# Kernel tuning notes

Hardware: AMD Instinct MI355X
Metric: run time of the kernel (lower is better)

The kernel has to match this reference:

```python
import jax, jax.numpy as jnp
import numpy as np


def sign_ste(x):
    # forward: sign(x); backward: grad * (|x| <= 1)  (straight-through estimator)
    # clip has exactly the STE gradient mask; stop_gradient swaps in sign(x) for fwd value.
    c = jnp.clip(x, -1.0, 1.0)
    return c + jax.lax.stop_gradient(jnp.sign(x) - c)


def setup_inputs() -> dict:
    key = jax.random.key(0)
    k1, k2, k3 = jax.random.split(key, 3)
    N, CIN, COUT = 8192, 4096, 4096
    input_x = jax.random.normal(k1, (N, CIN), dtype=jnp.float32)
    weight = jax.random.normal(k2, (COUT, CIN), dtype=jnp.float32) * 0.02
    bias = jax.random.normal(k3, (COUT,), dtype=jnp.float32) * 0.01
    return {"input_x": input_x, "weight": weight, "bias": bias}


def reference(input_x, weight, bias):
    qw = sign_ste(weight)            # [COUT, CIN], values in {-1, 0, +1}
    qx = sign_ste(input_x)           # [N, CIN]
    out = jnp.einsum('nc,oc->no', qx, qw)  # binary GEMM executed as float matmul
    alpha = jnp.mean(jnp.abs(weight))
    betta = jnp.mean(jnp.abs(input_x))
    return out * alpha * betta + bias
```

## Files before the change

### kernel.cpp

```cpp
#include <hip/hip_runtime.h>
#include <stdint.h>

#define N_ROWS 8192
#define C_IN   4096
#define C_OUT  4096
#define NCHUNK (C_IN / 64)
#define MT4    65536

typedef int   v4i  __attribute__((ext_vector_type(4)));
typedef int   v8i  __attribute__((ext_vector_type(8)));
typedef float v16f __attribute__((ext_vector_type(16)));

__global__ void pack_all_kernel(const float* __restrict__ x,
                                const float* __restrict__ w,
                                uint8_t* __restrict__ xf,
                                uint8_t* __restrict__ wf,
                                float* __restrict__ partials) {
    __shared__ __align__(16) uint16_t tile16[4096];
    __shared__ float sacc[4];

    const int b = blockIdx.x;
    const float* src; uint8_t* dst; int slab;
    if (b < 2048) { src = x; dst = xf; slab = b; }
    else          { src = w; dst = wf; slab = b - 2048; }
    const int mt = slab >> 3, cg = slab & 7;

    const int t = threadIdx.x;
    const int r = t >> 3, lc = t & 7;

    const float4* base = (const float4*)(src + (size_t)(mt * 32 + r) * C_IN + cg * 512) + lc;
    float acc = 0.f;
#pragma unroll
    for (int it = 0; it < 16; ++it) {
        float4 v = base[it * 8];
        uint16_t nv = (uint16_t)((v.x > 0.f ? 0x2u : 0xAu)
                               | (v.y > 0.f ? 0x2u : 0xAu) << 4
                               | (v.z > 0.f ? 0x2u : 0xAu) << 8
                               | (v.w > 0.f ? 0x2u : 0xAu) << 12);
        acc += fabsf(v.x) + fabsf(v.y) + fabsf(v.z) + fabsf(v.w);
        tile16[it * 256 + t] = nv;
    }
    __syncthreads();
    uint4* gout = (uint4*)(dst + (size_t)mt * MT4 + (size_t)cg * 8192);
    const uint4* lin = (const uint4*)tile16;
#pragma unroll
    for (int p = 0; p < 2; ++p) gout[p * 256 + t] = lin[p * 256 + t];

    for (int off = 32; off > 0; off >>= 1) acc += __shfl_down(acc, off, 64);
    const int lane = t & 63, wv = t >> 6;
    if (lane == 0) sacc[wv] = acc;
    __syncthreads();
    if (t == 0) {
        float s = 0.f;
        for (int i = 0; i < 4; ++i) s += sacc[i];
        partials[b] = s;
    }
}

__global__ void finalize_kernel(const float* __restrict__ part_x, int nx,
                                const float* __restrict__ part_w, int nw,
                                float* __restrict__ out_ab) {
    __shared__ float s[256];
    float ax = 0.f;
    for (int i = threadIdx.x; i < nx; i += 256) ax += part_x[i];
    s[threadIdx.x] = ax; __syncthreads();
    for (int st = 128; st > 0; st >>= 1) {
        if (threadIdx.x < st) s[threadIdx.x] += s[threadIdx.x + st];
        __syncthreads();
    }
    float sumx = s[0];
    __syncthreads();
    float aw = 0.f;
    for (int i = threadIdx.x; i < nw; i += 256) aw += part_w[i];
    s[threadIdx.x] = aw; __syncthreads();
    for (int st = 128; st > 0; st >>= 1) {
        if (threadIdx.x < st) s[threadIdx.x] += s[threadIdx.x + st];
        __syncthreads();
    }
    if (threadIdx.x == 0) {
        float sumw = s[0];
        float alpha = sumw / (float)((long long)C_OUT * C_IN);
        float betta = sumx / (float)((long long)N_ROWS * C_IN);
        out_ab[0] = alpha * betta;
    }
}

#define MF(a, b, c) \
    __builtin_amdgcn_mfma_scale_f32_32x32x64_f8f6f4( \
        __builtin_shufflevector((a), (a), 0, 1, 2, 3, -1, -1, -1, -1), \
        __builtin_shufflevector((b), (b), 0, 1, 2, 3, -1, -1, -1, -1), \
        (c), 4, 4, 0, 127, 0, 127)

__launch_bounds__(512, 2)
__global__ void xnor_gemm_fp4(const uint8_t* __restrict__ Afrag,
                              const uint8_t* __restrict__ Bfrag,
                              const float* __restrict__ bias,
                              const float* __restrict__ ab_ptr,
                              float* __restrict__ out) {
    __shared__ __align__(16) uint8_t lds[4][2][8192];

    const int t    = threadIdx.x;
    const int lane = t & 63;
    const int hi   = lane >> 5;
    const int r    = lane & 31;
    const int wid  = t >> 6;
    const int wr   = wid >> 2;
    const int wc   = wid & 3;

    const int id  = blockIdx.x;
    const int swz = (id & 7) * 64 + (id >> 3);
    const int brow = (swz >> 4) * 256;
    const int bcol = (swz & 15) * 256;

    const uint8_t* Abase = Afrag + (size_t)(brow >> 5) * MT4;
    const uint8_t* Bbase = Bfrag + (size_t)(bcol >> 5) * MT4;
    const size_t soff = (size_t)(t >> 6) * MT4 + (size_t)(t & 63) * 16;

#define STG(BUF, c)                                                                     \
    do {                                                                                \
        size_t ka = (size_t)(c) * 1024;                                                 \
        __builtin_amdgcn_global_load_lds(                                               \
            (const __attribute__((address_space(1))) void*)(Abase + soff + ka),         \
            (__attribute__((address_space(3))) void*)(&lds[BUF][0][t * 16]), 16, 0, 0); \
        __builtin_amdgcn_global_load_lds(                                               \
            (const __attribute__((address_space(1))) void*)(Bbase + soff + ka),         \
            (__attribute__((address_space(3))) void*)(&lds[BUF][1][t * 16]), 16, 0, 0); \
    } while (0)

#define LOADFRAGS(AS, BS, BUF)                                                       \
    do {                                                                             \
        AS[0] = *(const v4i*)(&lds[BUF][0][((wr * 4 + 0) * 64 + lane) * 16]);        \
        AS[1] = *(const v4i*)(&lds[BUF][0][((wr * 4 + 1) * 64 + lane) * 16]);        \
        AS[2] = *(const v4i*)(&lds[BUF][0][((wr * 4 + 2) * 64 + lane) * 16]);        \
        AS[3] = *(const v4i*)(&lds[BUF][0][((wr * 4 + 3) * 64 + lane) * 16]);        \
        BS[0] = *(const v4i*)(&lds[BUF][1][((wc * 2 + 0) * 64 + lane) * 16]);        \
        BS[1] = *(const v4i*)(&lds[BUF][1][((wc * 2 + 1) * 64 + lane) * 16]);        \
    } while (0)

#define DOMFMA(AS, BS)                                \
    do {                                              \
        acc[0][0] = MF(AS[0], BS[0], acc[0][0]);      \
        acc[0][1] = MF(AS[0], BS[1], acc[0][1]);      \
        acc[1][0] = MF(AS[1], BS[0], acc[1][0]);      \
        acc[1][1] = MF(AS[1], BS[1], acc[1][1]);      \
        acc[2][0] = MF(AS[2], BS[0], acc[2][0]);      \
        acc[2][1] = MF(AS[2], BS[1], acc[2][1]);      \
        acc[3][0] = MF(AS[3], BS[0], acc[3][0]);      \
        acc[3][1] = MF(AS[3], BS[1], acc[3][1]);      \
    } while (0)

#define BODY(cexp, SBUF, NBUF, CA, CB, NA, NB)                                      \
    do {                                                                            \
        const int c_ = (cexp);                                                      \
        if (c_ + 3 < NCHUNK) STG(SBUF, c_ + 3);                                     \
        if (c_ + 1 < NCHUNK) {                                                      \
            if (c_ < NCHUNK - 3)       { asm volatile("s_waitcnt vmcnt(4)" ::: "memory"); } \
            else if (c_ == NCHUNK - 3) { asm volatile("s_waitcnt vmcnt(2)" ::: "memory"); } \
            else                       { asm volatile("s_waitcnt vmcnt(0)" ::: "memory"); } \
        }                                                                           \
        asm volatile("s_waitcnt lgkmcnt(0)" ::: "memory");                          \
        __builtin_amdgcn_s_barrier();                                               \
        if (c_ + 1 < NCHUNK) LOADFRAGS(NA, NB, NBUF);                               \
        __builtin_amdgcn_s_setprio(1);                                              \
        DOMFMA(CA, CB);                                                             \
        __builtin_amdgcn_s_setprio(0);                                              \
    } while (0)

    v16f acc[4][2] = {};
    v4i A0[4], B0[2], A1[4], B1[2];

    STG(0, 0); STG(1, 1); STG(2, 2);
    asm volatile("s_waitcnt vmcnt(4)" ::: "memory");
    __builtin_amdgcn_s_barrier();
    LOADFRAGS(A0, B0, 0);

    for (int cb = 0; cb < NCHUNK; cb += 4) {
        BODY(cb + 0, 3, 1, A0, B0, A1, B1);
        BODY(cb + 1, 0, 2, A1, B1, A0, B0);
        BODY(cb + 2, 1, 3, A0, B0, A1, B1);
        BODY(cb + 3, 2, 0, A1, B1, A0, B0);
    }

    const float ab = ab_ptr[0];
#pragma unroll
    for (int m = 0; m < 4; ++m) {
#pragma unroll
        for (int n = 0; n < 2; ++n) {
            int col = bcol + wc * 64 + n * 32 + r;
            float bv = bias[col];
#pragma unroll
            for (int reg = 0; reg < 16; ++reg) {
                int rowf = (reg & 3) + 8 * (reg >> 2) + 4 * hi;
                int grow = brow + wr * 128 + m * 32 + rowf;
                out[(size_t)grow * C_OUT + col] = acc[m][n][reg] * ab + bv;
            }
        }
    }
#undef STG
#undef LOADFRAGS
#undef DOMFMA
#undef BODY
}

extern "C" void kernel_launch(void* const* d_in, const int* in_sizes, int n_in,
                              void* d_out, int out_size, void* d_ws, size_t ws_size,
                              hipStream_t stream) {
    const float* x    = (const float*)d_in[0];
    const float* w    = (const float*)d_in[1];
    const float* bias = (const float*)d_in[2];
    float* out = (float*)d_out;

    char* ws = (char*)d_ws;
    float* red      = (float*)ws;
    float* partials = red + 16;
    uint8_t* xs  = (uint8_t*)(ws + 16384);
    uint8_t* wsg = xs + (size_t)N_ROWS * C_IN / 2;

    pack_all_kernel<<<3072, 256, 0, stream>>>(x, w, xs, wsg, partials);
    finalize_kernel<<<1, 256, 0, stream>>>(partials, 2048, partials + 2048, 1024, red);

    dim3 grid((N_ROWS / 256) * (C_OUT / 256));
    xnor_gemm_fp4<<<grid, 512, 0, stream>>>(xs, wsg, bias, red, out);
}
```

Measured before the change: 140.2 us.

## Load MFMA fragments directly from global memory, dropping LDS staging

Removes the 4-stage LDS ring buffer and its global_load_lds staging, waitcnt and barriers. Each wave now loads its own A/B fp4 fragments straight from global memory into registers, double-buffered across k-chunks. This eliminates LDS traffic and block-wide synchronisation. In exchange, A and B tiles are reloaded from global/L2 by every wave that shares them (A by 4 waves, B by 2), and the prefetch depth drops to one chunk, so load latency may be exposed.

```diff
diff --git a/kernel.cpp b/kernel.cpp
--- a/kernel.cpp
+++ b/kernel.cpp
@@ -97,8 +97,6 @@
                               const float* __restrict__ bias,
                               const float* __restrict__ ab_ptr,
                               float* __restrict__ out) {
-    __shared__ __align__(16) uint8_t lds[4][2][8192];
-
     const int t    = threadIdx.x;
     const int lane = t & 63;
     const int hi   = lane >> 5;
@@ -112,33 +110,28 @@
     const int brow = (swz >> 4) * 256;
     const int bcol = (swz & 15) * 256;
 
-    const uint8_t* Abase = Afrag + (size_t)(brow >> 5) * MT4;
-    const uint8_t* Bbase = Bfrag + (size_t)(bcol >> 5) * MT4;
-    const size_t soff = (size_t)(t >> 6) * MT4 + (size_t)(t & 63) * 16;
+    const uint8_t* pa[4];
+    const uint8_t* pb[2];
+#pragma unroll
+    for (int m = 0; m < 4; ++m)
+        pa[m] = Afrag + (size_t)((brow >> 5) + wr * 4 + m) * MT4 + (size_t)lane * 16;
+#pragma unroll
+    for (int n = 0; n < 2; ++n)
+        pb[n] = Bfrag + (size_t)((bcol >> 5) + wc * 2 + n) * MT4 + (size_t)lane * 16;
 
-#define STG(BUF, c)                                                                     \
-    do {                                                                                \
-        size_t ka = (size_t)(c) * 1024;                                                 \
-        __builtin_amdgcn_global_load_lds(                                               \
-            (const __attribute__((address_space(1))) void*)(Abase + soff + ka),         \
-            (__attribute__((address_space(3))) void*)(&lds[BUF][0][t * 16]), 16, 0, 0); \
-        __builtin_amdgcn_global_load_lds(                                               \
-            (const __attribute__((address_space(1))) void*)(Bbase + soff + ka),         \
-            (__attribute__((address_space(3))) void*)(&lds[BUF][1][t * 16]), 16, 0, 0); \
-    } while (0)
-
-#define LOADFRAGS(AS, BS, BUF)                                                       \
-    do {                                                                             \
-        AS[0] = *(const v4i*)(&lds[BUF][0][((wr * 4 + 0) * 64 + lane) * 16]);        \
-        AS[1] = *(const v4i*)(&lds[BUF][0][((wr * 4 + 1) * 64 + lane) * 16]);        \
-        AS[2] = *(const v4i*)(&lds[BUF][0][((wr * 4 + 2) * 64 + lane) * 16]);        \
-        AS[3] = *(const v4i*)(&lds[BUF][0][((wr * 4 + 3) * 64 + lane) * 16]);        \
-        BS[0] = *(const v4i*)(&lds[BUF][1][((wc * 2 + 0) * 64 + lane) * 16]);        \
-        BS[1] = *(const v4i*)(&lds[BUF][1][((wc * 2 + 1) * 64 + lane) * 16]);        \
+#define LOADSET(AS, BS, c)                                                  \
+    do {                                                                    \
+        AS[0] = *(const v4i*)(pa[0] + (size_t)(c) * 1024);                  \
+        AS[1] = *(const v4i*)(pa[1] + (size_t)(c) * 1024);                  \
+        AS[2] = *(const v4i*)(pa[2] + (size_t)(c) * 1024);                  \
+        AS[3] = *(const v4i*)(pa[3] + (size_t)(c) * 1024);                  \
+        BS[0] = *(const v4i*)(pb[0] + (size_t)(c) * 1024);                  \
+        BS[1] = *(const v4i*)(pb[1] + (size_t)(c) * 1024);                  \
     } while (0)
 
 #define DOMFMA(AS, BS)                                \
     do {                                              \
+        __builtin_amdgcn_s_setprio(1);                \
         acc[0][0] = MF(AS[0], BS[0], acc[0][0]);      \
         acc[0][1] = MF(AS[0], BS[1], acc[0][1]);      \
         acc[1][0] = MF(AS[1], BS[0], acc[1][0]);      \
@@ -147,38 +140,19 @@
         acc[2][1] = MF(AS[2], BS[1], acc[2][1]);      \
         acc[3][0] = MF(AS[3], BS[0], acc[3][0]);      \
         acc[3][1] = MF(AS[3], BS[1], acc[3][1]);      \
-    } while (0)
-
-#define BODY(cexp, SBUF, NBUF, CA, CB, NA, NB)                                      \
-    do {                                                                            \
-        const int c_ = (cexp);                                                      \
-        if (c_ + 3 < NCHUNK) STG(SBUF, c_ + 3);                                     \
-        if (c_ + 1 < NCHUNK) {                                                      \
-            if (c_ < NCHUNK - 3)       { asm volatile("s_waitcnt vmcnt(4)" ::: "memory"); } \
-            else if (c_ == NCHUNK - 3) { asm volatile("s_waitcnt vmcnt(2)" ::: "memory"); } \
-            else                       { asm volatile("s_waitcnt vmcnt(0)" ::: "memory"); } \
-        }                                                                           \
-        asm volatile("s_waitcnt lgkmcnt(0)" ::: "memory");                          \
-        __builtin_amdgcn_s_barrier();                                               \
-        if (c_ + 1 < NCHUNK) LOADFRAGS(NA, NB, NBUF);                               \
-        __builtin_amdgcn_s_setprio(1);                                              \
-        DOMFMA(CA, CB);                                                             \
-        __builtin_amdgcn_s_setprio(0);                                              \
+        __builtin_amdgcn_s_setprio(0);                \
     } while (0)
 
     v16f acc[4][2] = {};
     v4i A0[4], B0[2], A1[4], B1[2];
 
-    STG(0, 0); STG(1, 1); STG(2, 2);
-    asm volatile("s_waitcnt vmcnt(4)" ::: "memory");
-    __builtin_amdgcn_s_barrier();
-    LOADFRAGS(A0, B0, 0);
+    LOADSET(A0, B0, 0);
 
-    for (int cb = 0; cb < NCHUNK; cb += 4) {
-        BODY(cb + 0, 3, 1, A0, B0, A1, B1);
-        BODY(cb + 1, 0, 2, A1, B1, A0, B0);
-        BODY(cb + 2, 1, 3, A0, B0, A1, B1);
-        BODY(cb + 3, 2, 0, A1, B1, A0, B0);
+    for (int cb = 0; cb < NCHUNK; cb += 2) {
+        LOADSET(A1, B1, cb + 1);
+        DOMFMA(A0, B0);
+        if (cb + 2 < NCHUNK) LOADSET(A0, B0, cb + 2);
+        DOMFMA(A1, B1);
     }
 
     const float ab = ab_ptr[0];
@@ -196,10 +170,8 @@
             }
         }
     }
-#undef STG
-#undef LOADFRAGS
+#undef LOADSET
 #undef DOMFMA
-#undef BODY
 }
 
 extern "C" void kernel_launch(void* const* d_in, const int* in_sizes, int n_in,
```

After: 147.3 us. 1.05x slower.

## Use 4 waves with 128x128 warp tiles and shorter prefetch depth in FP4 GEMM

Applied to the files above, without the earlier changes.

The GEMM block drops from 8 waves to 4 waves while keeping the 256x256 block tile, so each wave now computes a 128x128 sub-tile (4x4 MFMA accumulators instead of 4x2). This raises the MFMA-to-LDS-read ratio per wave. The global-to-LDS pipeline is cut from three chunks in flight to two, with each thread issuing four async loads per chunk, and a sched_barrier is added before the workgroup barrier. The cost is much higher accumulator register pressure (256 VGPRs for acc) and fewer waves to hide latency.

```diff
diff --git a/kernel.cpp b/kernel.cpp
--- a/kernel.cpp
+++ b/kernel.cpp
@@ -8,7 +8,6 @@
 #define MT4    65536
 
 typedef int   v4i  __attribute__((ext_vector_type(4)));
-typedef int   v8i  __attribute__((ext_vector_type(8)));
 typedef float v16f __attribute__((ext_vector_type(16)));
 
 __global__ void pack_all_kernel(const float* __restrict__ x,
@@ -91,21 +90,21 @@
         __builtin_shufflevector((b), (b), 0, 1, 2, 3, -1, -1, -1, -1), \
         (c), 4, 4, 0, 127, 0, 127)
 
-__launch_bounds__(512, 2)
+__launch_bounds__(256, 1)
 __global__ void xnor_gemm_fp4(const uint8_t* __restrict__ Afrag,
                               const uint8_t* __restrict__ Bfrag,
                               const float* __restrict__ bias,
                               const float* __restrict__ ab_ptr,
                               float* __restrict__ out) {
-    __shared__ __align__(16) uint8_t lds[4][2][8192];
+    __shared__ __align__(16) uint8_t lds[4][16384];
 
     const int t    = threadIdx.x;
     const int lane = t & 63;
     const int hi   = lane >> 5;
     const int r    = lane & 31;
     const int wid  = t >> 6;
-    const int wr   = wid >> 2;
-    const int wc   = wid & 3;
+    const int wr   = wid >> 1;
+    const int wc   = wid & 1;
 
     const int id  = blockIdx.x;
     const int swz = (id & 7) * 64 + (id >> 3);
@@ -114,79 +113,95 @@
 
     const uint8_t* Abase = Afrag + (size_t)(brow >> 5) * MT4;
     const uint8_t* Bbase = Bfrag + (size_t)(bcol >> 5) * MT4;
-    const size_t soff = (size_t)(t >> 6) * MT4 + (size_t)(t & 63) * 16;
-
-#define STG(BUF, c)                                                                     \
-    do {                                                                                \
-        size_t ka = (size_t)(c) * 1024;                                                 \
-        __builtin_amdgcn_global_load_lds(                                               \
-            (const __attribute__((address_space(1))) void*)(Abase + soff + ka),         \
-            (__attribute__((address_space(3))) void*)(&lds[BUF][0][t * 16]), 16, 0, 0); \
-        __builtin_amdgcn_global_load_lds(                                               \
-            (const __attribute__((address_space(1))) void*)(Bbase + soff + ka),         \
-            (__attribute__((address_space(3))) void*)(&lds[BUF][1][t * 16]), 16, 0, 0); \
-    } while (0)
-
-#define LOADFRAGS(AS, BS, BUF)                                                       \
-    do {                                                                             \
-        AS[0] = *(const v4i*)(&lds[BUF][0][((wr * 4 + 0) * 64 + lane) * 16]);        \
-        AS[1] = *(const v4i*)(&lds[BUF][0][((wr * 4 + 1) * 64 + lane) * 16]);        \
-        AS[2] = *(const v4i*)(&lds[BUF][0][((wr * 4 + 2) * 64 + lane) * 16]);        \
-        AS[3] = *(const v4i*)(&lds[BUF][0][((wr * 4 + 3) * 64 + lane) * 16]);        \
-        BS[0] = *(const v4i*)(&lds[BUF][1][((wc * 2 + 0) * 64 + lane) * 16]);        \
-        BS[1] = *(const v4i*)(&lds[BUF][1][((wc * 2 + 1) * 64 + lane) * 16]);        \
-    } while (0)
-
-#define DOMFMA(AS, BS)                                \
-    do {                                              \
-        acc[0][0] = MF(AS[0], BS[0], acc[0][0]);      \
-        acc[0][1] = MF(AS[0], BS[1], acc[0][1]);      \
-        acc[1][0] = MF(AS[1], BS[0], acc[1][0]);      \
-        acc[1][1] = MF(AS[1], BS[1], acc[1][1]);      \
-        acc[2][0] = MF(AS[2], BS[0], acc[2][0]);      \
-        acc[2][1] = MF(AS[2], BS[1], acc[2][1]);      \
-        acc[3][0] = MF(AS[3], BS[0], acc[3][0]);      \
-        acc[3][1] = MF(AS[3], BS[1], acc[3][1]);      \
-    } while (0)
-
-#define BODY(cexp, SBUF, NBUF, CA, CB, NA, NB)                                      \
+    const size_t soff0 = (size_t)(t >> 6) * MT4 + (size_t)(t & 63) * 16;
+    const size_t soff1 = soff0 + 4 * (size_t)MT4;
+
+#define STG(BUF, c)                                                                          \
+    do {                                                                                     \
+        size_t ka = (size_t)(c) * 1024;                                                      \
+        __builtin_amdgcn_global_load_lds(                                                    \
+            (const __attribute__((address_space(1))) void*)(Abase + soff0 + ka),             \
+            (__attribute__((address_space(3))) void*)(&lds[BUF][t * 16]), 16, 0, 0);         \
+        __builtin_amdgcn_global_load_lds(                                                    \
+            (const __attribute__((address_space(1))) void*)(Abase + soff1 + ka),             \
+            (__attribute__((address_space(3))) void*)(&lds[BUF][4096 + t * 16]), 16, 0, 0);  \
+        __builtin_amdgcn_global_load_lds(                                                    \
+            (const __attribute__((address_space(1))) void*)(Bbase + soff0 + ka),             \
+            (__attribute__((address_space(3))) void*)(&lds[BUF][8192 + t * 16]), 16, 0, 0);  \
+        __builtin_amdgcn_global_load_lds(                                                    \
+            (const __attribute__((address_space(1))) void*)(Bbase + soff1 + ka),             \
+            (__attribute__((address_space(3))) void*)(&lds[BUF][12288 + t * 16]), 16, 0, 0); \
+    } while (0)
+
+#define LOADFRAGS(AS, BS, BUF)                                                   \
+    do {                                                                         \
+        AS[0] = *(const v4i*)(&lds[BUF][(wr * 4 + 0) * 1024 + lane * 16]);       \
+        AS[1] = *(const v4i*)(&lds[BUF][(wr * 4 + 1) * 1024 + lane * 16]);       \
+        AS[2] = *(const v4i*)(&lds[BUF][(wr * 4 + 2) * 1024 + lane * 16]);       \
+        AS[3] = *(const v4i*)(&lds[BUF][(wr * 4 + 3) * 1024 + lane * 16]);       \
+        BS[0] = *(const v4i*)(&lds[BUF][8192 + (wc * 4 + 0) * 1024 + lane * 16]); \
+        BS[1] = *(const v4i*)(&lds[BUF][8192 + (wc * 4 + 1) * 1024 + lane * 16]); \
+        BS[2] = *(const v4i*)(&lds[BUF][8192 + (wc * 4 + 2) * 1024 + lane * 16]); \
+        BS[3] = *(const v4i*)(&lds[BUF][8192 + (wc * 4 + 3) * 1024 + lane * 16]); \
+    } while (0)
+
+#define DOMFMA(AS, BS)                                                     \
+    do {                                                                   \
+        __builtin_amdgcn_s_setprio(1);                                     \
+        acc[0][0] = MF(AS[0], BS[0], acc[0][0]);                           \
+        acc[0][1] = MF(AS[0], BS[1], acc[0][1]);                           \
+        acc[0][2] = MF(AS[0], BS[2], acc[0][2]);                           \
+        acc[0][3] = MF(AS[0], BS[3], acc[0][3]);                           \
+        acc[1][0] = MF(AS[1], BS[0], acc[1][0]);                           \
+        acc[1][1] = MF(AS[1], BS[1], acc[1][1]);                           \
+        acc[1][2] = MF(AS[1], BS[2], acc[1][2]);                           \
+        acc[1][3] = MF(AS[1], BS[3], acc[1][3]);                           \
+        acc[2][0] = MF(AS[2], BS[0], acc[2][0]);                           \
+        acc[2][1] = MF(AS[2], BS[1], acc[2][1]);                           \
+        acc[2][2] = MF(AS[2], BS[2], acc[2][2]);                           \
+        acc[2][3] = MF(AS[2], BS[3], acc[2][3]);                           \
+        acc[3][0] = MF(AS[3], BS[0], acc[3][0]);                           \
+        acc[3][1] = MF(AS[3], BS[1], acc[3][1]);                           \
+        acc[3][2] = MF(AS[3], BS[2], acc[3][2]);                           \
+        acc[3][3] = MF(AS[3], BS[3], acc[3][3]);                           \
+        __builtin_amdgcn_s_setprio(0);                                     \
+    } while (0)
+
+#define BODY(cexp, CA, CB, NA, NB)                                                  \
     do {                                                                            \
         const int c_ = (cexp);                                                      \
-        if (c_ + 3 < NCHUNK) STG(SBUF, c_ + 3);                                     \
-        if (c_ + 1 < NCHUNK) {                                                      \
-            if (c_ < NCHUNK - 3)       { asm volatile("s_waitcnt vmcnt(4)" ::: "memory"); } \
-            else if (c_ == NCHUNK - 3) { asm volatile("s_waitcnt vmcnt(2)" ::: "memory"); } \
-            else                       { asm volatile("s_waitcnt vmcnt(0)" ::: "memory"); } \
+        if (c_ + 2 < NCHUNK) {                                                      \
+            STG((c_ + 2) & 3, c_ + 2);                                              \
+            asm volatile("s_waitcnt vmcnt(4)" ::: "memory");                        \
+        } else {                                                                    \
+            asm volatile("s_waitcnt vmcnt(0)" ::: "memory");                        \
         }                                                                           \
         asm volatile("s_waitcnt lgkmcnt(0)" ::: "memory");                          \
+        __builtin_amdgcn_sched_barrier(0);                                          \
         __builtin_amdgcn_s_barrier();                                               \
-        if (c_ + 1 < NCHUNK) LOADFRAGS(NA, NB, NBUF);                               \
-        __builtin_amdgcn_s_setprio(1);                                              \
+        if (c_ + 1 < NCHUNK) LOADFRAGS(NA, NB, (c_ + 1) & 3);                       \
         DOMFMA(CA, CB);                                                             \
-        __builtin_amdgcn_s_setprio(0);                                              \
-    } while (0)
-
-    v16f acc[4][2] = {};
-    v4i A0[4], B0[2], A1[4], B1[2];
-
-    STG(0, 0); STG(1, 1); STG(2, 2);
+    } while (0)
+
+    v16f acc[4][4] = {};
+    v4i A0[4], B0[4], A1[4], B1[4];
+
+    STG(0, 0); STG(1, 1);
     asm volatile("s_waitcnt vmcnt(4)" ::: "memory");
     __builtin_amdgcn_s_barrier();
     LOADFRAGS(A0, B0, 0);
 
-    for (int cb = 0; cb < NCHUNK; cb += 4) {
-        BODY(cb + 0, 3, 1, A0, B0, A1, B1);
-        BODY(cb + 1, 0, 2, A1, B1, A0, B0);
-        BODY(cb + 2, 1, 3, A0, B0, A1, B1);
-        BODY(cb + 3, 2, 0, A1, B1, A0, B0);
+    for (int cb = 0; cb < NCHUNK; cb += 2) {
+        BODY(cb + 0, A0, B0, A1, B1);
+        BODY(cb + 1, A1, B1, A0, B0);
     }
 
     const float ab = ab_ptr[0];
 #pragma unroll
     for (int m = 0; m < 4; ++m) {
 #pragma unroll
-        for (int n = 0; n < 2; ++n) {
-            int col = bcol + wc * 64 + n * 32 + r;
+        for (int n = 0; n < 4; ++n) {
+            int col = bcol + wc * 128 + n * 32 + r;
             float bv = bias[col];
 #pragma unroll
             for (int reg = 0; reg < 16; ++reg) {
@@ -220,5 +235,5 @@
     finalize_kernel<<<1, 256, 0, stream>>>(partials, 2048, partials + 2048, 1024, red);
 
     dim3 grid((N_ROWS / 256) * (C_OUT / 256));
-    xnor_gemm_fp4<<<grid, 512, 0, stream>>>(xs, wsg, bias, red, out);
-}
+    xnor_gemm_fp4<<<grid, 256, 0, stream>>>(xs, wsg, bias, red, out);
+}
```

New measurement: 294.1 us. 110% more time.
